# Kernel tuning notes

Measured on AMD Instinct MI355X. Metric: run time of the kernel, lower is better.

The kernel has to match this reference:

```python
import jax, jax.numpy as jnp
import numpy as np

N_NODE = 40000
DIM = 128
N_REL = 8
N_EDGES = 640000
HOP = 2
BS = 128
SQLEN = 50
STDV = 1.0 / np.sqrt(DIM)
LEAKY_SLOPE = 0.2


def setup_inputs() -> dict:
    key = jax.random.key(0)
    ks = jax.random.split(key, 12)
    inputs = jax.random.randint(ks[0], (BS, SQLEN), 0, N_NODE)
    A = jax.random.randint(ks[1], (BS, SQLEN, SQLEN), 0, 5)  # edge types 0..4
    mask_item = jnp.ones((BS, SQLEN), dtype=jnp.int32)
    embedding = jax.random.normal(ks[2], (N_NODE, DIM), jnp.float32) * STDV
    r_embed_w = jax.random.normal(ks[3], (N_REL, DIM), jnp.float32) * STDV
    trans_M = jax.random.normal(ks[4], (N_REL, DIM, DIM), jnp.float32) * STDV
    a_0 = jax.random.normal(ks[5], (DIM, 1), jnp.float32) * STDV
    a_1 = jax.random.normal(ks[6], (DIM, 1), jnp.float32) * STDV
    a_2 = jax.random.normal(ks[7], (DIM, 1), jnp.float32) * STDV
    a_3 = jax.random.normal(ks[8], (DIM, 1), jnp.float32) * STDV
    a_in_values = jax.random.uniform(ks[9], (N_EDGES,), jnp.float32)
    h_list = jax.random.randint(ks[10], (N_EDGES,), 0, N_NODE, dtype=jnp.int32)
    t_list = jax.random.randint(ks[11], (N_EDGES,), 0, N_NODE, dtype=jnp.int32)
    return {"inputs": inputs, "A": A, "mask_item": mask_item,
            "embedding": embedding, "r_embed_w": r_embed_w, "trans_M": trans_M,
            "a_0": a_0, "a_1": a_1, "a_2": a_2, "a_3": a_3,
            "a_in_values": a_in_values, "h_list": h_list, "t_list": t_list}


def local_agg(h, adj, a_stack):
    # h: (B,N,D); adj: (B,N,N) int codes; a_stack: (4,D)
    pair = h[:, :, None, :] * h[:, None, :, :]            # (B,N,N,D) pairwise product
    pair = jnp.where(pair > 0, pair, LEAKY_SLOPE * pair)  # LeakyReLU
    e = jnp.einsum('bijd,kd->bijk', pair, a_stack)        # 4 attention logits per pair
    alpha = jnp.full(e.shape[:-1], -9e15, e.dtype)
    for k in range(4):
        alpha = jnp.where(adj == k + 1, e[..., k], alpha)
    alpha = jax.nn.softmax(alpha, axis=-1)
    return jnp.einsum('bij,bjd->bid', alpha, h)


def spmm(v, rows, cols, x):
    # (sparse A) @ x with COO (rows, cols, v)
    return jax.ops.segment_sum(v[:, None] * x[cols], rows, num_segments=x.shape[0])


def sparse_row_softmax(v, rows, n):
    m = jax.ops.segment_max(v, rows, num_segments=n)
    e = jnp.exp(v - m[rows])
    s = jax.ops.segment_sum(e, rows, num_segments=n)
    return e / s[rows]


def update_attention(ego, h_list, t_list, trans_M, r_emb):
    # edges are block-sorted by relation with equal counts per relation
    per = h_list.shape[0] // N_REL
    vals = []
    for r in range(N_REL):
        sl = slice(r * per, (r + 1) * per)
        W = trans_M[r]                      # (D,D) TransR projection
        r_mul_h = ego[h_list[sl]] @ W
        r_mul_t = ego[t_list[sl]] @ W
        vals.append(jnp.sum(jnp.tanh(r_mul_t) * r_mul_h + r_emb[r], axis=1))
    return jnp.concatenate(vals)


def forward_fn(embedding, r_embed_w, trans_M, a_0, a_1, a_2, a_3,
               a_in_values, inputs, A, h_list, t_list):
    origin = embedding
    ego = embedding
    v = a_in_values
    all_embed = []
    for k in range(HOP):
        ego = spmm(v, h_list, t_list, ego)  # Aggregator (dropout in eval = identity)
        all_embed.append(ego)
        if k < HOP - 1:
            v_new = update_attention(ego, h_list, t_list, trans_M, r_embed_w)
            # torch assigns via .data with requires_grad=False -> constant
            v = jax.lax.stop_gradient(sparse_row_softmax(v_new, h_list, N_NODE))
    kg = sum(all_embed) / HOP
    a_stack = jnp.concatenate([a_0, a_1, a_2, a_3], axis=1).T  # (4,D)
    node_embeds = origin[inputs]            # (B,N,D)
    hidden = local_agg(node_embeds, A, a_stack)
    kg_embeds = kg[inputs]
    hidden = hidden + local_agg(kg_embeds, A, a_stack)
    return hidden, node_embeds


def reference(inputs, A, mask_item, embedding, r_embed_w, trans_M,
              a_0, a_1, a_2, a_3, a_in_values, h_list, t_list):
    return forward_fn(embedding, r_embed_w, trans_M, a_0, a_1, a_2, a_3,
                      a_in_values, inputs, A, h_list, t_list)
```

## Files before the change

kernel.cpp:

```cpp
#include <hip/hip_runtime.h>

#define N_NODE  40000
#define DIM     128
#define N_REL   8
#define N_EDGES 640000
#define PER_REL (N_EDGES / N_REL)
#define BS      128
#define SQ      50
#define NB      ((N_NODE + 255) / 256)
#define RSPLIT  8
#define RPB     (N_REL / RSPLIT)
#define CONVB   ((N_NODE * 64) / 256)
#define HISTB   (N_EDGES / 1024)

typedef unsigned int        u32;
typedef unsigned short      u16;
typedef unsigned long long  u64;
typedef short  bf16x8 __attribute__((ext_vector_type(8)));
typedef float  f32x4  __attribute__((ext_vector_type(4)));
typedef u32    u32x4  __attribute__((ext_vector_type(4)));

__device__ __forceinline__ u16 f2bf(float f) {
  union { float f; u32 i; } c; c.f = f;
  u32 b = c.i;
  b += 0x7FFFu + ((b >> 16) & 1u);
  return (u16)(b >> 16);
}
__device__ __forceinline__ float bf2f(u32 u) {
  union { u32 i; float f; } c; c.i = u << 16; return c.f;
}
__device__ __forceinline__ float bflo(u32 w) {
  union { u32 i; float f; } c; c.i = w << 16; return c.f;
}
__device__ __forceinline__ float bfhi(u32 w) {
  union { u32 i; float f; } c; c.i = w & 0xffff0000u; return c.f;
}
__device__ __forceinline__ u32 pk2(float a, float b) {
  return (u32)f2bf(a) | ((u32)f2bf(b) << 16);
}
__device__ __forceinline__ float tanh_fast(float x) {
  float e = __expf(2.f * x);
  return 1.f - 2.f * __builtin_amdgcn_rcpf(e + 1.f);
}

__global__ void __launch_bounds__(256)
prep_kernel(const float* __restrict__ emb, u32* __restrict__ embb,
            const float* __restrict__ W, u16* __restrict__ Wtb,
            const float* __restrict__ rembw, float* __restrict__ rsum8,
            const int* __restrict__ hl, int* __restrict__ cnt,
            int* __restrict__ rank) {
  int bid = blockIdx.x;
  if (bid < CONVB) {
    int i = bid * 256 + threadIdx.x;
    float2 v = reinterpret_cast<const float2*>(emb)[i];
    embb[i] = pk2(v.x, v.y);
  } else if (bid < CONVB + HISTB) {
    int base = (bid - CONVB) * 1024 + threadIdx.x;
    int hn[4], rk[4];
    #pragma unroll
    for (int j = 0; j < 4; j++) hn[j] = hl[base + j * 256];
    #pragma unroll
    for (int j = 0; j < 4; j++) rk[j] = atomicAdd(&cnt[hn[j]], 1);
    #pragma unroll
    for (int j = 0; j < 4; j++) rank[base + j * 256] = rk[j];
  } else if (bid < CONVB + HISTB + N_REL) {
    int r = bid - CONVB - HISTB;
    const float* Wr = W + (size_t)r * DIM * DIM;
    u16* o = Wtb + (size_t)r * DIM * DIM;
    for (int x = threadIdx.x; x < DIM * DIM; x += 256) {
      int n = x >> 7, k = x & 127;
      o[x] = f2bf(Wr[k * DIM + n]);
    }
  } else {
    int wv = threadIdx.x >> 6, lane = threadIdx.x & 63;
    for (int r = wv; r < N_REL; r += 4) {
      float s = rembw[r * DIM + lane] + rembw[r * DIM + 64 + lane];
      #pragma unroll
      for (int o = 32; o; o >>= 1) s += __shfl_xor(s, o, 64);
      if (lane == 0) rsum8[r] = s;
    }
  }
}

__global__ void bsum_kernel(const int* __restrict__ cnt, int* __restrict__ bsum) {
  __shared__ int sd[256];
  int i = blockIdx.x * 256 + threadIdx.x;
  sd[threadIdx.x] = (i < N_NODE) ? cnt[i] : 0;
  __syncthreads();
  for (int o = 128; o; o >>= 1) {
    if (threadIdx.x < o) sd[threadIdx.x] += sd[threadIdx.x + o];
    __syncthreads();
  }
  if (!threadIdx.x) bsum[blockIdx.x] = sd[0];
}

__global__ void scan_bsum_kernel(int* __restrict__ bsum) {
  __shared__ int sd[256];
  int t = threadIdx.x;
  int orig = (t < NB) ? bsum[t] : 0;
  sd[t] = orig;
  __syncthreads();
  for (int o = 1; o < 256; o <<= 1) {
    int v = (t >= o) ? sd[t - o] : 0;
    __syncthreads();
    sd[t] += v;
    __syncthreads();
  }
  if (t < NB) bsum[t] = sd[t] - orig;
}

__global__ void scan_final_kernel(const int* __restrict__ cnt, const int* __restrict__ bsum,
                                  int* __restrict__ rowptr) {
  __shared__ int sd[256];
  int t = threadIdx.x;
  int i = blockIdx.x * 256 + t;
  int orig = (i < N_NODE) ? cnt[i] : 0;
  sd[t] = orig;
  __syncthreads();
  for (int o = 1; o < 256; o <<= 1) {
    int v = (t >= o) ? sd[t - o] : 0;
    __syncthreads();
    sd[t] += v;
    __syncthreads();
  }
  int ex = sd[t] - orig + bsum[blockIdx.x];
  if (i < N_NODE) {
    rowptr[i] = ex;
    if (i == N_NODE - 1) rowptr[N_NODE] = ex + orig;
  }
}

__global__ void __launch_bounds__(256)
scatter_kernel(const int* __restrict__ hl, const int* __restrict__ tl,
               const float* __restrict__ ain, const int* __restrict__ rowptr,
               const int* __restrict__ rank, u64* __restrict__ pay64) {
  int base = blockIdx.x * 1024 + threadIdx.x;
  int pos[4];
  u64 pl[4];
  #pragma unroll
  for (int j = 0; j < 4; j++) {
    int e = base + j * 256;
    int hn = hl[e];
    pos[j] = rowptr[hn] + rank[e];
    int r = e / PER_REL;
    u32 lo = (u32)tl[e] | ((u32)hn << 16);
    u32 hi = (u32)r | ((u32)f2bf(ain[e]) << 16);
    pl[j] = ((u64)hi << 32) | lo;
  }
  #pragma unroll
  for (int j = 0; j < 4; j++) pay64[pos[j]] = pl[j];
}

__global__ void __launch_bounds__(256)
spmm_pay0(const u32* __restrict__ xb, const u64* __restrict__ pay64,
          const int* __restrict__ rowptr, u32* __restrict__ outb) {
  int row = (blockIdx.x * 256 + threadIdx.x) >> 6;
  if (row >= N_NODE) return;
  int lane = threadIdx.x & 63;
  int lo = rowptr[row], n = rowptr[row + 1] - lo;
  float ax = 0.f, ay = 0.f;
  const u32* xl = xb + lane;
  int p = 0;
  for (; p + 7 < n; p += 8) {
    u64 q[8]; u32 w[8];
    #pragma unroll
    for (int j = 0; j < 8; j++) q[j] = pay64[lo + p + j];
    #pragma unroll
    for (int j = 0; j < 8; j++) w[j] = xl[(size_t)((u32)q[j] & 0xffffu) << 6];
    #pragma unroll
    for (int j = 0; j < 8; j++) {
      float v = bf2f((u32)(q[j] >> 48));
      ax += v * bflo(w[j]);
      ay += v * bfhi(w[j]);
    }
  }
  for (; p < n; p++) {
    u64 q0 = pay64[lo + p];
    float v0 = bf2f((u32)(q0 >> 48));
    u32 w0 = xl[(size_t)((u32)q0 & 0xffffu) << 6];
    ax += v0 * bflo(w0);
    ay += v0 * bfhi(w0);
  }
  outb[((size_t)row << 6) + lane] = pk2(ax, ay);
}

__global__ void __launch_bounds__(256)
score_spmm(const u16* __restrict__ projb_all, const u32* __restrict__ xb,
           const u64* __restrict__ pay64, const int* __restrict__ rowptr,
           const float* __restrict__ rsum8, float* __restrict__ vals,
           u32* __restrict__ outb) {
  int row = (blockIdx.x * 256 + threadIdx.x) >> 6;
  if (row >= N_NODE) return;
  int lane = threadIdx.x & 63;
  int g = lane >> 4, le = lane & 15;
  int lo = rowptr[row], n = rowptr[row + 1] - lo;

  float gsum = 0.f;
  for (int p0 = 0; p0 < n; p0 += 4) {
    int p = p0 + g;
    bool valid = p < n;
    int t = 0, r = 0;
    if (valid) {
      u64 q = pay64[lo + p];
      t = (int)((u32)q & 0xffffu);
      r = (int)((u32)(q >> 32) & 0xffu);
    }
    float s = 0.f;
    if (valid) {
      const u16* base = projb_all + (size_t)r * N_NODE * DIM;
      bf16x8 tv = *reinterpret_cast<const bf16x8*>(base + (size_t)t * DIM + le * 8);
      bf16x8 hv = *reinterpret_cast<const bf16x8*>(base + (size_t)row * DIM + le * 8);
      const u32* tw = reinterpret_cast<const u32*>(&tv);
      const u32* hw = reinterpret_cast<const u32*>(&hv);
      #pragma unroll
      for (int i = 0; i < 4; i++) {
        s += tanh_fast(bflo(tw[i])) * bflo(hw[i]);
        s += tanh_fast(bf2f(tw[i] >> 16)) * bfhi(hw[i]);
      }
    }
    #pragma unroll
    for (int o = 8; o; o >>= 1) s += __shfl_xor(s, o, 64);
    if (valid && le == 0) {
      float e = __expf(s + rsum8[r]);
      vals[lo + p] = e;
      gsum += e;
    }
  }
  float rs = (le == 0) ? gsum : 0.f;
  #pragma unroll
  for (int o = 32; o; o >>= 1) rs += __shfl_xor(rs, o, 64);
  float inv = (rs > 0.f) ? 1.f / rs : 0.f;

  float ax = 0.f, ay = 0.f;
  const u32* xl = xb + lane;
  int p = 0;
  for (; p + 7 < n; p += 8) {
    u32 w[8]; float v[8];
    #pragma unroll
    for (int j = 0; j < 8; j++) v[j] = vals[lo + p + j];
    #pragma unroll
    for (int j = 0; j < 8; j++)
      w[j] = xl[(size_t)((u32)pay64[lo + p + j] & 0xffffu) << 6];
    #pragma unroll
    for (int j = 0; j < 8; j++) {
      ax += v[j] * bflo(w[j]);
      ay += v[j] * bfhi(w[j]);
    }
  }
  for (; p < n; p++) {
    float v0 = vals[lo + p];
    u32 w0 = xl[(size_t)((u32)pay64[lo + p] & 0xffffu) << 6];
    ax += v0 * bflo(w0);
    ay += v0 * bfhi(w0);
  }
  outb[((size_t)row << 6) + lane] = pk2(ax * inv, ay * inv);
}

__global__ void __launch_bounds__(256)
proj_mfma4(const u32* __restrict__ egob, const u16* __restrict__ Wtb,
           u16* __restrict__ projb_all) {
  __shared__ u16 Buf[128 * 136];
  int tid = threadIdx.x;
  int rel0  = (blockIdx.x & (RSPLIT - 1)) * RPB;
  int gbase = (blockIdx.x / RSPLIT) * 128;

  for (int x = tid; x < 128 * 64; x += 256) {
    int m = x >> 6, d2 = x & 63;
    int gm = gbase + m; if (gm >= N_NODE) gm = N_NODE - 1;
    u32 v = egob[((size_t)gm << 6) + d2];
    int byte = (m * 256 + d2 * 4) ^ ((m & 7) << 4);
    *reinterpret_cast<u32*>(reinterpret_cast<char*>(Buf) + byte) = v;
  }
  __syncthreads();

  int w = tid >> 6, lane = tid & 63;
  int l15 = lane & 15, g = lane >> 4;

  bf16x8 afr[2][4];
  #pragma unroll
  for (int kk = 0; kk < 4; kk++) {
    int kb = (kk * 32 + g * 8) * 2;
    #pragma unroll
    for (int mt = 0; mt < 2; mt++) {
      int m = w * 32 + mt * 16 + l15;
      int byte = (m * 256 + kb) ^ ((m & 7) << 4);
      afr[mt][kk] = *reinterpret_cast<bf16x8*>(reinterpret_cast<char*>(Buf) + byte);
    }
  }
  __syncthreads();

  for (int rr = 0; rr < RPB; rr++) {
    int r = rel0 + rr;
    const u32* Wr32 = reinterpret_cast<const u32*>(Wtb + (size_t)r * DIM * DIM);
    for (int x = tid; x < 128 * 64; x += 256) {
      int n = x >> 6, k2 = x & 63;
      int byte = (n * 256 + k2 * 4) ^ ((n & 7) << 4);
      *reinterpret_cast<u32*>(reinterpret_cast<char*>(Buf) + byte) = Wr32[x];
    }
    __syncthreads();

    f32x4 acc[2][8];
    #pragma unroll
    for (int mt = 0; mt < 2; mt++)
      #pragma unroll
      for (int nt = 0; nt < 8; nt++) acc[mt][nt] = (f32x4){0.f, 0.f, 0.f, 0.f};

    #pragma unroll
    for (int kk = 0; kk < 4; kk++) {
      int kb = (kk * 32 + g * 8) * 2;
      #pragma unroll
      for (int nt = 0; nt < 8; nt++) {
        int n = nt * 16 + l15;
        int byte = (n * 256 + kb) ^ ((n & 7) << 4);
        bf16x8 b = *reinterpret_cast<bf16x8*>(reinterpret_cast<char*>(Buf) + byte);
        acc[0][nt] = __builtin_amdgcn_mfma_f32_16x16x32_bf16(afr[0][kk], b, acc[0][nt], 0, 0, 0);
        acc[1][nt] = __builtin_amdgcn_mfma_f32_16x16x32_bf16(afr[1][kk], b, acc[1][nt], 0, 0, 0);
      }
    }
    __syncthreads();

    #pragma unroll
    for (int mt = 0; mt < 2; mt++)
      #pragma unroll
      for (int reg = 0; reg < 4; reg++) {
        int row = w * 32 + mt * 16 + g * 4 + reg;
        #pragma unroll
        for (int nt = 0; nt < 8; nt++)
          Buf[row * 136 + nt * 16 + l15] = f2bf(acc[mt][nt][reg]);
      }
    __syncthreads();

    const u32x4* Cs = reinterpret_cast<const u32x4*>(Buf);
    u32* dst = reinterpret_cast<u32*>(projb_all + (size_t)r * N_NODE * DIM);
    for (int x = tid; x < 128 * 16; x += 256) {
      int row = x >> 4, q = x & 15;
      int node = gbase + row;
      if (node < N_NODE) {
        u32x4 v = Cs[row * 17 + q];
        *reinterpret_cast<u32x4*>(dst + ((size_t)node << 6) + q * 4) = v;
      }
    }
    __syncthreads();
  }
}

__global__ void __launch_bounds__(512)
local_agg4(const float* __restrict__ emb, const u32* __restrict__ ego1b,
           const u32* __restrict__ ego2b, const int* __restrict__ inp,
           const int* __restrict__ Aadj,
           const float* __restrict__ a0, const float* __restrict__ a1,
           const float* __restrict__ a2, const float* __restrict__ a3,
           float* __restrict__ out_hidden, float* __restrict__ out_node,
           float* __restrict__ tmpK) {
  __shared__ u16   Qb[64 * 256];
  __shared__ u16   hTb[128 * 64];
  __shared__ float aC[4][256];
  __shared__ float S[4][64 * 66];
  __shared__ u16   P[64 * 64];
  __shared__ float sinv[64];
  __shared__ int   adjL[SQ * SQ];

  int b = blockIdx.x >> 1, which = blockIdx.x & 1;
  int tid = threadIdx.x;

  {
    int k = tid >> 7, d = tid & 127;
    const float* ap = (k == 0) ? a0 : (k == 1) ? a1 : (k == 2) ? a2 : a3;
    float av = ap[d];
    aC[k][d] = 0.6f * av;
    aC[k][128 + d] = 0.4f * av;
  }
  for (int x = tid; x < SQ * SQ; x += 512) adjL[x] = Aadj[b * SQ * SQ + x];
  for (int x = tid; x < 128 * 16; x += 512) {
    int d = x >> 4, j = 48 + (x & 15);
    if (j >= 50) {
      int byte = (d * 128 + j * 2) ^ ((d & 7) << 4);
      *reinterpret_cast<u16*>(reinterpret_cast<char*>(hTb) + byte) = 0;
    }
  }
  for (int x = tid; x < SQ * 64; x += 512) {
    int j = x >> 6, d2 = (x & 63) << 1;
    int node = inp[b * SQ + j];
    float v0, v1;
    if (which == 0) {
      float2 vv = *reinterpret_cast<const float2*>(emb + (size_t)node * DIM + d2);
      v0 = vv.x; v1 = vv.y;
      *reinterpret_cast<float2*>(out_node + (size_t)(b * SQ + j) * DIM + d2) = vv;
    } else {
      u32 w1 = ego1b[((size_t)node << 6) + (d2 >> 1)];
      u32 w2 = ego2b[((size_t)node << 6) + (d2 >> 1)];
      v0 = 0.5f * (bf2f(w1 & 0xffffu) + bf2f(w2 & 0xffffu));
      v1 = 0.5f * (bf2f(w1 >> 16) + bf2f(w2 >> 16));
    }
    u16 b0 = f2bf(v0), b1 = f2bf(v1);
    { int byte = (j * 512 + d2 * 2) ^ ((j & 7) << 4);
      *reinterpret_cast<u32*>(reinterpret_cast<char*>(Qb) + byte) = (u32)b0 | ((u32)b1 << 16); }
    { int byte = (j * 512 + 256 + d2 * 2) ^ ((j & 7) << 4);
      u32 m0 = b0 & 0x7fffu, m1 = b1 & 0x7fffu;
      *reinterpret_cast<u32*>(reinterpret_cast<char*>(Qb) + byte) = m0 | (m1 << 16); }
    { int byte = (d2 * 128 + j * 2) ^ ((d2 & 7) << 4);
      *reinterpret_cast<u16*>(reinterpret_cast<char*>(hTb) + byte) = b0; }
    { int byte = ((d2 + 1) * 128 + j * 2) ^ (((d2 + 1) & 7) << 4);
      *reinterpret_cast<u16*>(reinterpret_cast<char*>(hTb) + byte) = b1; }
  }
  __syncthreads();

  int w = tid >> 6, lane = tid & 63;
  int l15 = lane & 15, g = lane >> 4;

  {
    int k = w >> 1, half = w & 1;
    const float* aCk = aC[k];
    f32x4 acc[2][4];
    #pragma unroll
    for (int mt = 0; mt < 2; mt++)
      #pragma unroll
      for (int nt = 0; nt < 4; nt++) acc[mt][nt] = (f32x4){0.f, 0.f, 0.f, 0.f};
    for (int ks = 0; ks < 8; ks++) {
      int kb = ks * 32 + g * 8;
      float4 c01 = *reinterpret_cast<const float4*>(aCk + kb);
      float4 c23 = *reinterpret_cast<const float4*>(aCk + kb + 4);
      bf16x8 afr[2];
      #pragma unroll
      for (int mt = 0; mt < 2; mt++) {
        int m = (half * 2 + mt) * 16 + l15;
        int byte = (m * 512 + kb * 2) ^ ((m & 7) << 4);
        union { bf16x8 v; u32 u[4]; } qv, o;
        qv.v = *reinterpret_cast<bf16x8*>(reinterpret_cast<char*>(Qb) + byte);
        o.u[0] = pk2(bf2f(qv.u[0] & 0xffffu) * c01.x, bf2f(qv.u[0] >> 16) * c01.y);
        o.u[1] = pk2(bf2f(qv.u[1] & 0xffffu) * c01.z, bf2f(qv.u[1] >> 16) * c01.w);
        o.u[2] = pk2(bf2f(qv.u[2] & 0xffffu) * c23.x, bf2f(qv.u[2] >> 16) * c23.y);
        o.u[3] = pk2(bf2f(qv.u[3] & 0xffffu) * c23.z, bf2f(qv.u[3] >> 16) * c23.w);
        afr[mt] = o.v;
      }
      #pragma unroll
      for (int nt = 0; nt < 4; nt++) {
        int n = nt * 16 + l15;
        int byte = (n * 512 + kb * 2) ^ ((n & 7) << 4);
        bf16x8 bfr = *reinterpret_cast<bf16x8*>(reinterpret_cast<char*>(Qb) + byte);
        acc[0][nt] = __builtin_amdgcn_mfma_f32_16x16x32_bf16(afr[0], bfr, acc[0][nt], 0, 0, 0);
        acc[1][nt] = __builtin_amdgcn_mfma_f32_16x16x32_bf16(afr[1], bfr, acc[1][nt], 0, 0, 0);
      }
    }
    #pragma unroll
    for (int mt = 0; mt < 2; mt++)
      #pragma unroll
      for (int nt = 0; nt < 4; nt++)
        #pragma unroll
        for (int reg = 0; reg < 4; reg++) {
          int m = (half * 2 + mt) * 16 + g * 4 + reg;
          int n = nt * 16 + l15;
          S[k][m * 66 + n] = acc[mt][nt][reg];
        }
  }
  __syncthreads();

  for (int i = w; i < SQ; i += 8) {
    float p = 0.f;
    if (lane < SQ) {
      int sel = adjL[i * SQ + lane];
      if (sel > 0) p = __expf(S[sel - 1][i * 66 + lane]);
    }
    float s = p;
    #pragma unroll
    for (int off = 32; off; off >>= 1) s += __shfl_xor(s, off, 64);
    if (lane == 0) sinv[i] = (s > 0.f) ? 1.f / s : 0.f;
    int byte = (i * 128 + lane * 2) ^ ((i & 7) << 4);
    *reinterpret_cast<u16*>(reinterpret_cast<char*>(P) + byte) = f2bf(p);
  }
  __syncthreads();

  {
    int mt = w >> 1, ng = w & 1;
    f32x4 acc[4];
    #pragma unroll
    for (int nt = 0; nt < 4; nt++) acc[nt] = (f32x4){0.f, 0.f, 0.f, 0.f};
    #pragma unroll
    for (int ks = 0; ks < 2; ks++) {
      int kb = ks * 32 + g * 8;
      int m = mt * 16 + l15;
      int abyte = (m * 128 + kb * 2) ^ ((m & 7) << 4);
      bf16x8 afr = *reinterpret_cast<bf16x8*>(reinterpret_cast<char*>(P) + abyte);
      #pragma unroll
      for (int nt = 0; nt < 4; nt++) {
        int d = (ng * 4 + nt) * 16 + l15;
        int byte = (d * 128 + kb * 2) ^ ((d & 7) << 4);
        bf16x8 bfr = *reinterpret_cast<bf16x8*>(reinterpret_cast<char*>(hTb) + byte);
        acc[nt] = __builtin_amdgcn_mfma_f32_16x16x32_bf16(afr, bfr, acc[nt], 0, 0, 0);
      }
    }
    float* dst = which ? tmpK : out_hidden;
    #pragma unroll
    for (int nt = 0; nt < 4; nt++)
      #pragma unroll
      for (int reg = 0; reg < 4; reg++) {
        int i = mt * 16 + g * 4 + reg;
        if (i < SQ) {
          int d = (ng * 4 + nt) * 16 + l15;
          dst[(size_t)(b * SQ + i) * DIM + d] = acc[nt][reg] * sinv[i];
        }
      }
  }
}

__global__ void add_kernel(float* __restrict__ out, const float* __restrict__ add) {
  int i = blockIdx.x * 256 + threadIdx.x;
  float4 a = reinterpret_cast<const float4*>(add)[i];
  float4 o = reinterpret_cast<float4*>(out)[i];
  o.x += a.x; o.y += a.y; o.z += a.z; o.w += a.w;
  reinterpret_cast<float4*>(out)[i] = o;
}

extern "C" void kernel_launch(void* const* d_in, const int* in_sizes, int n_in,
                              void* d_out, int out_size, void* d_ws, size_t ws_size,
                              hipStream_t stream) {
  const int*   inputs = (const int*)d_in[0];
  const int*   Aadj   = (const int*)d_in[1];
  const float* emb    = (const float*)d_in[3];
  const float* rembw  = (const float*)d_in[4];
  const float* transM = (const float*)d_in[5];
  const float* a0     = (const float*)d_in[6];
  const float* a1     = (const float*)d_in[7];
  const float* a2     = (const float*)d_in[8];
  const float* a3     = (const float*)d_in[9];
  const float* ain    = (const float*)d_in[10];
  const int*   hl     = (const int*)d_in[11];
  const int*   tl     = (const int*)d_in[12];

  u32*   ego1b    = (u32*)d_ws;
  u32*   ego2b    = ego1b + (size_t)N_NODE * 64;
  u32*   embb     = ego2b + (size_t)N_NODE * 64;
  u16*   projball = (u16*)(embb + (size_t)N_NODE * 64);
  u16*   Wtb      = projball + (size_t)N_REL * N_NODE * DIM;
  u64*   pay64    = (u64*)(Wtb + (size_t)N_REL * DIM * DIM);
  float* vals     = (float*)(pay64 + N_EDGES);
  int*   rank     = (int*)(vals + N_EDGES);
  int*   cnt      = rank + N_EDGES;
  int*   rowptr   = cnt + N_NODE;
  int*   bsum     = rowptr + N_NODE + 64;
  float* rsum8    = (float*)(bsum + 256);
  float* tmpK     = rsum8 + 64;

  float* out_hidden = (float*)d_out;
  float* out_node   = out_hidden + (size_t)BS * SQ * DIM;

  hipMemsetAsync(cnt, 0, N_NODE * sizeof(int), stream);
  prep_kernel<<<CONVB + HISTB + N_REL + 1, 256, 0, stream>>>(
      emb, embb, transM, Wtb, rembw, rsum8, hl, cnt, rank);
  bsum_kernel<<<NB, 256, 0, stream>>>(cnt, bsum);
  scan_bsum_kernel<<<1, 256, 0, stream>>>(bsum);
  scan_final_kernel<<<NB, 256, 0, stream>>>(cnt, bsum, rowptr);
  scatter_kernel<<<N_EDGES / 1024, 256, 0, stream>>>(hl, tl, ain, rowptr, rank, pay64);

  spmm_pay0<<<(N_NODE * 64) / 256, 256, 0, stream>>>(embb, pay64, rowptr, ego1b);

  proj_mfma4<<<((N_NODE + 127) / 128) * RSPLIT, 256, 0, stream>>>(ego1b, Wtb, projball);

  score_spmm<<<(N_NODE * 64) / 256, 256, 0, stream>>>(projball, ego1b, pay64, rowptr,
                                                      rsum8, vals, ego2b);

  local_agg4<<<BS * 2, 512, 0, stream>>>(emb, ego1b, ego2b, inputs, Aadj,
                                         a0, a1, a2, a3, out_hidden, out_node, tmpK);
  add_kernel<<<(BS * SQ * DIM / 4) / 256, 256, 0, stream>>>(out_hidden, tmpK);
}
```

Measured before the change: 229.7 us.

## Store relation projections as fp8 with precomputed tanh to cut gather bytes

```diff
diff --git a/kernel.cpp b/kernel.cpp
--- a/kernel.cpp
+++ b/kernel.cpp
@@ -15,10 +15,19 @@
 
 typedef unsigned int        u32;
 typedef unsigned short      u16;
+typedef unsigned char       u8;
 typedef unsigned long long  u64;
 typedef short  bf16x8 __attribute__((ext_vector_type(8)));
 typedef float  f32x4  __attribute__((ext_vector_type(4)));
+typedef float  f32x2  __attribute__((ext_vector_type(2)));
 typedef u32    u32x4  __attribute__((ext_vector_type(4)));
+
+#if __has_builtin(__builtin_amdgcn_cvt_pk_f32_fp8)
+#define HW_FP8_DEC 1
+#endif
+#if __has_builtin(__builtin_amdgcn_cvt_pk_fp8_f32)
+#define HW_FP8_ENC 1
+#endif
 
 __device__ __forceinline__ u16 f2bf(float f) {
   union { float f; u32 i; } c; c.f = f;
@@ -41,6 +50,46 @@
 __device__ __forceinline__ float tanh_fast(float x) {
   float e = __expf(2.f * x);
   return 1.f - 2.f * __builtin_amdgcn_rcpf(e + 1.f);
+}
+
+__device__ __forceinline__ u32 f2fp8(float f) {
+  union { float f; u32 i; } c; c.f = f;
+  u32 b = c.i;
+  u32 s = (b >> 24) & 0x80u;
+  u32 mag = b & 0x7fffffffu;
+  mag += 0x7FFFFu + ((mag >> 20) & 1u);
+  int e8 = (int)(mag >> 23) - 120;
+  if (e8 >= 16) return s | 0x7Eu;
+  if (e8 <= 0) {
+    float af = fabsf(f) * 512.f + 0.5f;
+    int m2 = (int)af;
+    if (m2 > 7) return s | 0x08u;
+    return s | (u32)m2;
+  }
+  return s | ((u32)e8 << 3) | ((mag >> 20) & 7u);
+}
+__device__ __forceinline__ float fp8d(u32 byte) {
+  u32 em = byte & 0x7fu;
+  u32 e  = em >> 3;
+  u32 M  = e ? (em & 7u) + 8u : em;
+  u32 E  = e ? e : 1u;
+  union { u32 i; float f; } sc; sc.i = (E + 117u) << 23;
+  float v = (float)M * sc.f;
+  return (byte & 0x80u) ? -v : v;
+}
+__device__ __forceinline__ float fp8dot4(u32 ta, u32 ha) {
+#ifdef HW_FP8_DEC
+  f32x2 t0 = __builtin_amdgcn_cvt_pk_f32_fp8(ta, 0);
+  f32x2 t1 = __builtin_amdgcn_cvt_pk_f32_fp8(ta, 1);
+  f32x2 h0 = __builtin_amdgcn_cvt_pk_f32_fp8(ha, 0);
+  f32x2 h1 = __builtin_amdgcn_cvt_pk_f32_fp8(ha, 1);
+  return t0.x * h0.x + t0.y * h0.y + t1.x * h1.x + t1.y * h1.y;
+#else
+  return fp8d(ta & 255u) * fp8d(ha & 255u)
+       + fp8d((ta >> 8) & 255u) * fp8d((ha >> 8) & 255u)
+       + fp8d((ta >> 16) & 255u) * fp8d((ha >> 16) & 255u)
+       + fp8d(ta >> 24) * fp8d(ha >> 24);
+#endif
 }
 
 __global__ void __launch_bounds__(256)
@@ -185,7 +234,7 @@
 }
 
 __global__ void __launch_bounds__(256)
-score_spmm(const u16* __restrict__ projb_all, const u32* __restrict__ xb,
+score_spmm(const u8* __restrict__ projf8, const u32* __restrict__ xb,
            const u64* __restrict__ pay64, const int* __restrict__ rowptr,
            const float* __restrict__ rsum8, float* __restrict__ vals,
            u32* __restrict__ outb) {
@@ -207,16 +256,12 @@
     }
     float s = 0.f;
     if (valid) {
-      const u16* base = projb_all + (size_t)r * N_NODE * DIM;
-      bf16x8 tv = *reinterpret_cast<const bf16x8*>(base + (size_t)t * DIM + le * 8);
-      bf16x8 hv = *reinterpret_cast<const bf16x8*>(base + (size_t)row * DIM + le * 8);
-      const u32* tw = reinterpret_cast<const u32*>(&tv);
-      const u32* hw = reinterpret_cast<const u32*>(&hv);
-      #pragma unroll
-      for (int i = 0; i < 4; i++) {
-        s += tanh_fast(bflo(tw[i])) * bflo(hw[i]);
-        s += tanh_fast(bf2f(tw[i] >> 16)) * bfhi(hw[i]);
-      }
+      const u8* base = projf8 + (size_t)r * N_NODE * 256;
+      const u32* tp = reinterpret_cast<const u32*>(base + (size_t)t * 256 + le * 8);
+      const u32* hp = reinterpret_cast<const u32*>(base + (size_t)row * 256 + 128 + le * 8);
+      u32 ta = tp[0], tb = tp[1];
+      u32 ha = hp[0], hb = hp[1];
+      s = fp8dot4(ta, ha) + fp8dot4(tb, hb);
     }
     #pragma unroll
     for (int o = 8; o; o >>= 1) s += __shfl_xor(s, o, 64);
@@ -258,7 +303,7 @@
 
 __global__ void __launch_bounds__(256)
 proj_mfma4(const u32* __restrict__ egob, const u16* __restrict__ Wtb,
-           u16* __restrict__ projb_all) {
+           u8* __restrict__ projf8) {
   __shared__ u16 Buf[128 * 136];
   int tid = threadIdx.x;
   int rel0  = (blockIdx.x & (RSPLIT - 1)) * RPB;
@@ -319,19 +364,31 @@
     }
     __syncthreads();
 
+    char* BufB = reinterpret_cast<char*>(Buf);
     #pragma unroll
     for (int mt = 0; mt < 2; mt++)
       #pragma unroll
       for (int reg = 0; reg < 4; reg++) {
         int row = w * 32 + mt * 16 + g * 4 + reg;
+        char* rb = BufB + row * 272;
         #pragma unroll
-        for (int nt = 0; nt < 8; nt++)
-          Buf[row * 136 + nt * 16 + l15] = f2bf(acc[mt][nt][reg]);
+        for (int nt = 0; nt < 8; nt++) {
+          float v = acc[mt][nt][reg];
+          int col = nt * 16 + l15;
+#ifdef HW_FP8_ENC
+          u32 pk = (u32)__builtin_amdgcn_cvt_pk_fp8_f32(tanh_fast(v), v, 0, 0);
+          rb[col]       = (char)(pk & 255u);
+          rb[128 + col] = (char)((pk >> 8) & 255u);
+#else
+          rb[col]       = (char)f2fp8(tanh_fast(v));
+          rb[128 + col] = (char)f2fp8(v);
+#endif
+        }
       }
     __syncthreads();
 
     const u32x4* Cs = reinterpret_cast<const u32x4*>(Buf);
-    u32* dst = reinterpret_cast<u32*>(projb_all + (size_t)r * N_NODE * DIM);
+    u32* dst = reinterpret_cast<u32*>(projf8 + (size_t)r * N_NODE * 256);
     for (int x = tid; x < 128 * 16; x += 256) {
       int row = x >> 4, q = x & 15;
       int node = gbase + row;
@@ -530,8 +587,8 @@
   u32*   ego1b    = (u32*)d_ws;
   u32*   ego2b    = ego1b + (size_t)N_NODE * 64;
   u32*   embb     = ego2b + (size_t)N_NODE * 64;
-  u16*   projball = (u16*)(embb + (size_t)N_NODE * 64);
-  u16*   Wtb      = projball + (size_t)N_REL * N_NODE * DIM;
+  u8*    projf8   = (u8*)(embb + (size_t)N_NODE * 64);
+  u16*   Wtb      = (u16*)(projf8 + (size_t)N_REL * N_NODE * 256);
   u64*   pay64    = (u64*)(Wtb + (size_t)N_REL * DIM * DIM);
   float* vals     = (float*)(pay64 + N_EDGES);
   int*   rank     = (int*)(vals + N_EDGES);
@@ -554,9 +611,9 @@
 
   spmm_pay0<<<(N_NODE * 64) / 256, 256, 0, stream>>>(embb, pay64, rowptr, ego1b);
 
-  proj_mfma4<<<((N_NODE + 127) / 128) * RSPLIT, 256, 0, stream>>>(ego1b, Wtb, projball);
-
-  score_spmm<<<(N_NODE * 64) / 256, 256, 0, stream>>>(projball, ego1b, pay64, rowptr,
+  proj_mfma4<<<((N_NODE + 127) / 128) * RSPLIT, 256, 0, stream>>>(ego1b, Wtb, projf8);
+
+  score_spmm<<<(N_NODE * 64) / 256, 256, 0, stream>>>(projf8, ego1b, pay64, rowptr,
                                                       rsum8, vals, ego2b);
 
   local_agg4<<<BS * 2, 512, 0, stream>>>(emb, ego1b, ego2b, inputs, Aadj,
```

Measured after the change: 227.3 us. No clear change (-1.0%).
